# Optimization experiments

Hardware: AMD Instinct MI355X
Metric: run time of the kernel (lower is better)

The kernel has to match this reference:

```python
import jax, jax.numpy as jnp
import numpy as np

VOXEL = 128
N_PTS = VOXEL ** 3  # 2,097,152
C_FEAT = 14
T_HASH = 4194304


def _hash_index(coords, table_size):
    # Instant-NGP style spatial hash: elementwise prime multiply, xor-reduce, mod T.
    # uint32 arithmetic emulates the wrap-around semantics of the integer hash.
    primes = jnp.array([1, 2654435761, 805459861], dtype=jnp.uint32)
    h = coords.astype(jnp.uint32) * primes  # [N, 3]
    return ((h[:, 0] ^ h[:, 1]) ^ h[:, 2]) % jnp.uint32(table_size)  # [N]


def _quat_to_rotmat(q):
    # q: [N, 4] normalized, (r, x, y, z) convention (standard 3DGS)
    r, x, y, z = q[:, 0], q[:, 1], q[:, 2], q[:, 3]
    R = jnp.stack([
        1 - 2 * (y * y + z * z), 2 * (x * y - r * z), 2 * (x * z + r * y),
        2 * (x * y + r * z), 1 - 2 * (x * x + z * z), 2 * (y * z - r * x),
        2 * (x * z - r * y), 2 * (y * z + r * x), 1 - 2 * (x * x + y * y),
    ], axis=-1)
    return R.reshape(-1, 3, 3)


def setup_inputs() -> dict:
    key = jax.random.key(0)
    k1, k2, k3 = jax.random.split(key, 3)
    coordinates = jax.random.randint(k1, (N_PTS, 3), 0, VOXEL, dtype=jnp.int32)
    hash_table = jax.random.normal(k2, (C_FEAT, T_HASH), dtype=jnp.float32)
    camera_center = jax.random.normal(k3, (3,), dtype=jnp.float32)
    far = jnp.ones((1,), dtype=jnp.float32)
    return {"coordinates": coordinates, "hash_table": hash_table,
            "camera_center": camera_center, "far": far, "voxel_size": VOXEL}


def reference(coordinates, hash_table, camera_center, far, voxel_size):
    far_s = far[0]
    vs = jnp.float32(voxel_size)

    # hash_query: [C, N] gather from hash table
    idx = _hash_index(coordinates, hash_table.shape[1])
    gf = hash_table[:, idx]  # [14, N]

    # compute_voxel_center: [N, 3]
    voxel_center = (coordinates.astype(jnp.float32) / vs * 2 * far_s
                    - far_s + camera_center[None, :] + far_s / vs)

    # delta means: normalize over ALL elements (torch.mean/std on full tensor, unbiased std)
    dm = gf[0:3].T  # [N, 3]
    dm = (dm - jnp.mean(dm)) / jnp.std(dm, ddof=1) * 2 * far_s / vs / 6.0
    means = dm + voxel_center  # [N, 3]

    # covariance from scaling + rotation (standard 3DGS)
    scales = jax.nn.sigmoid(gf[7:10].T) * 2 * far_s / vs  # [N, 3]
    q = gf[3:7].T
    q = q / jnp.linalg.norm(q, axis=-1, keepdims=True)
    R = _quat_to_rotmat(q)                       # [N, 3, 3]
    L = R * scales[:, None, :]                   # L = R @ diag(s)
    covariances = jnp.einsum('nij,nkj->nik', L, L)  # [N, 3, 3]

    harmonics = gf[10:13].T[:, :, None]          # [N, 3, 1] (raw features)
    opacities = jax.nn.sigmoid(gf[13] - 4.0)     # [N]

    n = coordinates.shape[0]
    return (means[None], covariances[None], harmonics[None], opacities[None])
```

## Files before the change

### kernel.cpp

```cpp
#include <hip/hip_runtime.h>
#include <math.h>

#define N_PTS (128*128*128)
#define T_HASH 4194304
#define T_MASK (T_HASH - 1)
#define ENTRY_STRIDE 16

__device__ __forceinline__ unsigned hash_idx(int x, int y, int z) {
    return ((unsigned)x ^ ((unsigned)y * 2654435761u)
                        ^ ((unsigned)z * 805459861u)) & T_MASK;
}

__global__ void transpose_kernel(const float* __restrict__ table,
                                 float* __restrict__ tt) {
    __shared__ float sh[256 * 17];
    const int t  = threadIdx.x;
    const int i0 = blockIdx.x * 256;

    #pragma unroll
    for (int j = 0; j < 14; ++j)
        sh[t * 17 + j] = table[(size_t)j * T_HASH + i0 + t];
    sh[t * 17 + 14] = 0.f;
    sh[t * 17 + 15] = 0.f;
    __syncthreads();

    float4* dst = (float4*)(tt + (size_t)i0 * ENTRY_STRIDE);
    #pragma unroll
    for (int k = 0; k < 4; ++k) {
        const int f = t + k * 256;
        const int p = f >> 2;
        const int c = f & 3;
        const float* s = &sh[p * 17 + c * 4];
        dst[f] = make_float4(s[0], s[1], s[2], s[3]);
    }
}

__global__ void reduce_kernel_t(const int* __restrict__ coords,
                                const float* __restrict__ tt,
                                double* __restrict__ acc) {
    float s = 0.f, ss = 0.f;
    const int stride = gridDim.x * blockDim.x;
    for (int i = blockIdx.x * blockDim.x + threadIdx.x; i < N_PTS; i += stride) {
        const unsigned idx = hash_idx(coords[i*3], coords[i*3+1], coords[i*3+2]);
        const float4 f = *(const float4*)(tt + (size_t)idx * ENTRY_STRIDE);
        s  += f.x + f.y + f.z;
        ss += f.x * f.x + f.y * f.y + f.z * f.z;
    }
    #pragma unroll
    for (int off = 32; off > 0; off >>= 1) {
        s  += __shfl_down(s, off, 64);
        ss += __shfl_down(ss, off, 64);
    }
    __shared__ float sh_s[4], sh_ss[4];
    const int lane = threadIdx.x & 63;
    const int wid  = threadIdx.x >> 6;
    if (lane == 0) { sh_s[wid] = s; sh_ss[wid] = ss; }
    __syncthreads();
    if (threadIdx.x == 0) {
        float ts = 0.f, tss = 0.f;
        for (int w = 0; w < 4; ++w) { ts += sh_s[w]; tss += sh_ss[w]; }
        atomicAdd(&acc[0], (double)ts);
        atomicAdd(&acc[1], (double)tss);
    }
}

__global__ void reduce_kernel_o(const int* __restrict__ coords,
                                const float* __restrict__ table,
                                double* __restrict__ acc) {
    float s = 0.f, ss = 0.f;
    const int stride = gridDim.x * blockDim.x;
    for (int i = blockIdx.x * blockDim.x + threadIdx.x; i < N_PTS; i += stride) {
        const unsigned idx = hash_idx(coords[i*3], coords[i*3+1], coords[i*3+2]);
        float g0 = table[idx];
        float g1 = table[T_HASH + idx];
        float g2 = table[2 * T_HASH + idx];
        s  += g0 + g1 + g2;
        ss += g0 * g0 + g1 * g1 + g2 * g2;
    }
    #pragma unroll
    for (int off = 32; off > 0; off >>= 1) {
        s  += __shfl_down(s, off, 64);
        ss += __shfl_down(ss, off, 64);
    }
    __shared__ float sh_s[4], sh_ss[4];
    const int lane = threadIdx.x & 63;
    const int wid  = threadIdx.x >> 6;
    if (lane == 0) { sh_s[wid] = s; sh_ss[wid] = ss; }
    __syncthreads();
    if (threadIdx.x == 0) {
        float ts = 0.f, tss = 0.f;
        for (int w = 0; w < 4; ++w) { ts += sh_s[w]; tss += sh_ss[w]; }
        atomicAdd(&acc[0], (double)ts);
        atomicAdd(&acc[1], (double)tss);
    }
}

template <bool TRANSPOSED>
__global__ void main_kernel(const int* __restrict__ coords,
                            const float* __restrict__ tab,
                            const float* __restrict__ cam,
                            const float* __restrict__ far_p,
                            const int* __restrict__ vs_p,
                            const double* __restrict__ acc,
                            float* __restrict__ out) {
    const int i = blockIdx.x * blockDim.x + threadIdx.x;
    if (i >= N_PTS) return;

    const float far_s = far_p[0];
    const float vs    = (float)vs_p[0];

    const double n      = 3.0 * (double)N_PTS;
    const double sum    = acc[0];
    const double sumsq  = acc[1];
    const double mean_d = sum / n;
    const double var_d  = (sumsq - sum * sum / n) / (n - 1.0);
    const float mean    = (float)mean_d;
    const float inv_std = (float)(1.0 / sqrt(var_d));

    const int cx = coords[i * 3 + 0];
    const int cy = coords[i * 3 + 1];
    const int cz = coords[i * 3 + 2];
    const unsigned idx = hash_idx(cx, cy, cz);

    float g[16];
    if (TRANSPOSED) {
        const float4* e = (const float4*)(tab + (size_t)idx * ENTRY_STRIDE);
        float4 f0 = e[0], f1 = e[1], f2 = e[2], f3 = e[3];
        g[0]=f0.x; g[1]=f0.y; g[2]=f0.z; g[3]=f0.w;
        g[4]=f1.x; g[5]=f1.y; g[6]=f1.z; g[7]=f1.w;
        g[8]=f2.x; g[9]=f2.y; g[10]=f2.z; g[11]=f2.w;
        g[12]=f3.x; g[13]=f3.y;
    } else {
        #pragma unroll
        for (int j = 0; j < 14; ++j)
            g[j] = tab[(size_t)j * T_HASH + idx];
    }

    const float two_far_over_vs = 2.f * far_s / vs;
    const float dm_scale = two_far_over_vs / 6.f;
    const float c_f[3] = { (float)cx, (float)cy, (float)cz };
    #pragma unroll
    for (int k = 0; k < 3; ++k) {
        const float vc = c_f[k] / vs * 2.f * far_s - far_s + cam[k] + far_s / vs;
        out[(size_t)i * 3 + k] = (g[k] - mean) * inv_std * dm_scale + vc;
    }

    float qr = g[3], qx = g[4], qy = g[5], qz = g[6];
    const float qinv = 1.f / sqrtf(qr * qr + qx * qx + qy * qy + qz * qz);
    qr *= qinv; qx *= qinv; qy *= qinv; qz *= qinv;

    float R[3][3];
    R[0][0] = 1.f - 2.f * (qy * qy + qz * qz);
    R[0][1] = 2.f * (qx * qy - qr * qz);
    R[0][2] = 2.f * (qx * qz + qr * qy);
    R[1][0] = 2.f * (qx * qy + qr * qz);
    R[1][1] = 1.f - 2.f * (qx * qx + qz * qz);
    R[1][2] = 2.f * (qy * qz - qr * qx);
    R[2][0] = 2.f * (qx * qz - qr * qy);
    R[2][1] = 2.f * (qy * qz + qr * qx);
    R[2][2] = 1.f - 2.f * (qx * qx + qy * qy);

    float sc[3];
    #pragma unroll
    for (int k = 0; k < 3; ++k)
        sc[k] = two_far_over_vs / (1.f + expf(-g[7 + k]));

    float* covp = out + (size_t)3 * N_PTS + (size_t)i * 9;
    #pragma unroll
    for (int r = 0; r < 3; ++r) {
        #pragma unroll
        for (int c = 0; c < 3; ++c) {
            float a = 0.f;
            #pragma unroll
            for (int j = 0; j < 3; ++j)
                a += (R[r][j] * sc[j]) * (R[c][j] * sc[j]);
            covp[r * 3 + c] = a;
        }
    }

    float* harp = out + (size_t)12 * N_PTS + (size_t)i * 3;
    #pragma unroll
    for (int k = 0; k < 3; ++k)
        harp[k] = g[10 + k];

    out[(size_t)15 * N_PTS + i] = 1.f / (1.f + expf(-(g[13] - 4.f)));
}

extern "C" void kernel_launch(void* const* d_in, const int* in_sizes, int n_in,
                              void* d_out, int out_size, void* d_ws, size_t ws_size,
                              hipStream_t stream) {
    const int*   coords = (const int*)d_in[0];
    const float* table  = (const float*)d_in[1];
    const float* cam    = (const float*)d_in[2];
    const float* far_p  = (const float*)d_in[3];
    const int*   vs_p   = (const int*)d_in[4];
    float*       out    = (float*)d_out;

    double* acc = (double*)d_ws;
    float*  tt  = (float*)((char*)d_ws + 256);

    const size_t need = 256 + (size_t)T_HASH * ENTRY_STRIDE * sizeof(float);

    hipMemsetAsync(d_ws, 0, 2 * sizeof(double), stream);

    const int threads = 256;
    const int blocks  = (N_PTS + threads - 1) / threads;

    if (ws_size >= need) {
        transpose_kernel<<<T_HASH / 256, 256, 0, stream>>>(table, tt);
        reduce_kernel_t<<<2048, 256, 0, stream>>>(coords, tt, acc);
        main_kernel<true><<<blocks, threads, 0, stream>>>(coords, tt, cam, far_p,
                                                          vs_p, acc, out);
    } else {
        reduce_kernel_o<<<2048, 256, 0, stream>>>(coords, table, acc);
        main_kernel<false><<<blocks, threads, 0, stream>>>(coords, table, cam,
                                                           far_p, vs_p, acc, out);
    }
}
```

Baseline: 543.6 us.

## Fuse statistics reduction into main gather kernel and fix up means afterwards

Removes the separate reduction pass that re-gathered the first three features for every point. The main kernel now writes raw delta-mean features and accumulates the sum and sum of squares per block. A small fixup kernel then normalizes the means using the global statistics. Most output stores become nontemporal. The workspace-size fallback path is dropped, so the code assumes the transposed table always fits.

```diff
diff --git a/kernel.cpp b/kernel.cpp
--- a/kernel.cpp
+++ b/kernel.cpp
@@ -35,117 +35,34 @@
     }
 }
 
-__global__ void reduce_kernel_t(const int* __restrict__ coords,
-                                const float* __restrict__ tt,
-                                double* __restrict__ acc) {
-    float s = 0.f, ss = 0.f;
-    const int stride = gridDim.x * blockDim.x;
-    for (int i = blockIdx.x * blockDim.x + threadIdx.x; i < N_PTS; i += stride) {
-        const unsigned idx = hash_idx(coords[i*3], coords[i*3+1], coords[i*3+2]);
-        const float4 f = *(const float4*)(tt + (size_t)idx * ENTRY_STRIDE);
-        s  += f.x + f.y + f.z;
-        ss += f.x * f.x + f.y * f.y + f.z * f.z;
-    }
-    #pragma unroll
-    for (int off = 32; off > 0; off >>= 1) {
-        s  += __shfl_down(s, off, 64);
-        ss += __shfl_down(ss, off, 64);
-    }
-    __shared__ float sh_s[4], sh_ss[4];
-    const int lane = threadIdx.x & 63;
-    const int wid  = threadIdx.x >> 6;
-    if (lane == 0) { sh_s[wid] = s; sh_ss[wid] = ss; }
-    __syncthreads();
-    if (threadIdx.x == 0) {
-        float ts = 0.f, tss = 0.f;
-        for (int w = 0; w < 4; ++w) { ts += sh_s[w]; tss += sh_ss[w]; }
-        atomicAdd(&acc[0], (double)ts);
-        atomicAdd(&acc[1], (double)tss);
-    }
-}
-
-__global__ void reduce_kernel_o(const int* __restrict__ coords,
-                                const float* __restrict__ table,
-                                double* __restrict__ acc) {
-    float s = 0.f, ss = 0.f;
-    const int stride = gridDim.x * blockDim.x;
-    for (int i = blockIdx.x * blockDim.x + threadIdx.x; i < N_PTS; i += stride) {
-        const unsigned idx = hash_idx(coords[i*3], coords[i*3+1], coords[i*3+2]);
-        float g0 = table[idx];
-        float g1 = table[T_HASH + idx];
-        float g2 = table[2 * T_HASH + idx];
-        s  += g0 + g1 + g2;
-        ss += g0 * g0 + g1 * g1 + g2 * g2;
-    }
-    #pragma unroll
-    for (int off = 32; off > 0; off >>= 1) {
-        s  += __shfl_down(s, off, 64);
-        ss += __shfl_down(ss, off, 64);
-    }
-    __shared__ float sh_s[4], sh_ss[4];
-    const int lane = threadIdx.x & 63;
-    const int wid  = threadIdx.x >> 6;
-    if (lane == 0) { sh_s[wid] = s; sh_ss[wid] = ss; }
-    __syncthreads();
-    if (threadIdx.x == 0) {
-        float ts = 0.f, tss = 0.f;
-        for (int w = 0; w < 4; ++w) { ts += sh_s[w]; tss += sh_ss[w]; }
-        atomicAdd(&acc[0], (double)ts);
-        atomicAdd(&acc[1], (double)tss);
-    }
-}
-
-template <bool TRANSPOSED>
-__global__ void main_kernel(const int* __restrict__ coords,
-                            const float* __restrict__ tab,
-                            const float* __restrict__ cam,
-                            const float* __restrict__ far_p,
-                            const int* __restrict__ vs_p,
-                            const double* __restrict__ acc,
-                            float* __restrict__ out) {
-    const int i = blockIdx.x * blockDim.x + threadIdx.x;
-    if (i >= N_PTS) return;
+__global__ void main_fused_kernel(const int* __restrict__ coords,
+                                  const float* __restrict__ tt,
+                                  const float* __restrict__ far_p,
+                                  const int* __restrict__ vs_p,
+                                  double* __restrict__ acc,
+                                  float* __restrict__ out) {
+    const int i = blockIdx.x * 256 + threadIdx.x;
 
     const float far_s = far_p[0];
     const float vs    = (float)vs_p[0];
-
-    const double n      = 3.0 * (double)N_PTS;
-    const double sum    = acc[0];
-    const double sumsq  = acc[1];
-    const double mean_d = sum / n;
-    const double var_d  = (sumsq - sum * sum / n) / (n - 1.0);
-    const float mean    = (float)mean_d;
-    const float inv_std = (float)(1.0 / sqrt(var_d));
+    const float two_far_over_vs = 2.f * far_s / vs;
 
     const int cx = coords[i * 3 + 0];
     const int cy = coords[i * 3 + 1];
     const int cz = coords[i * 3 + 2];
     const unsigned idx = hash_idx(cx, cy, cz);
 
-    float g[16];
-    if (TRANSPOSED) {
-        const float4* e = (const float4*)(tab + (size_t)idx * ENTRY_STRIDE);
-        float4 f0 = e[0], f1 = e[1], f2 = e[2], f3 = e[3];
-        g[0]=f0.x; g[1]=f0.y; g[2]=f0.z; g[3]=f0.w;
-        g[4]=f1.x; g[5]=f1.y; g[6]=f1.z; g[7]=f1.w;
-        g[8]=f2.x; g[9]=f2.y; g[10]=f2.z; g[11]=f2.w;
-        g[12]=f3.x; g[13]=f3.y;
-    } else {
-        #pragma unroll
-        for (int j = 0; j < 14; ++j)
-            g[j] = tab[(size_t)j * T_HASH + idx];
-    }
+    const float4* e = (const float4*)(tt + (size_t)idx * ENTRY_STRIDE);
+    const float4 f0 = e[0];
+    const float4 f1 = e[1];
+    const float4 f2 = e[2];
+    const float4 f3 = e[3];
 
-    const float two_far_over_vs = 2.f * far_s / vs;
-    const float dm_scale = two_far_over_vs / 6.f;
-    const float c_f[3] = { (float)cx, (float)cy, (float)cz };
-    #pragma unroll
-    for (int k = 0; k < 3; ++k) {
-        const float vc = c_f[k] / vs * 2.f * far_s - far_s + cam[k] + far_s / vs;
-        out[(size_t)i * 3 + k] = (g[k] - mean) * inv_std * dm_scale + vc;
-    }
+    out[(size_t)i * 3 + 0] = f0.x;
+    out[(size_t)i * 3 + 1] = f0.y;
+    out[(size_t)i * 3 + 2] = f0.z;
 
-    float qr = g[3], qx = g[4], qy = g[5], qz = g[6];
+    float qr = f0.w, qx = f1.x, qy = f1.y, qz = f1.z;
     const float qinv = 1.f / sqrtf(qr * qr + qx * qx + qy * qy + qz * qz);
     qr *= qinv; qx *= qinv; qy *= qinv; qz *= qinv;
 
@@ -161,9 +78,9 @@
     R[2][2] = 1.f - 2.f * (qx * qx + qy * qy);
 
     float sc[3];
-    #pragma unroll
-    for (int k = 0; k < 3; ++k)
-        sc[k] = two_far_over_vs / (1.f + expf(-g[7 + k]));
+    sc[0] = two_far_over_vs / (1.f + expf(-f1.w));
+    sc[1] = two_far_over_vs / (1.f + expf(-f2.x));
+    sc[2] = two_far_over_vs / (1.f + expf(-f2.y));
 
     float* covp = out + (size_t)3 * N_PTS + (size_t)i * 9;
     #pragma unroll
@@ -174,16 +91,73 @@
             #pragma unroll
             for (int j = 0; j < 3; ++j)
                 a += (R[r][j] * sc[j]) * (R[c][j] * sc[j]);
-            covp[r * 3 + c] = a;
+            __builtin_nontemporal_store(a, covp + r * 3 + c);
         }
     }
 
     float* harp = out + (size_t)12 * N_PTS + (size_t)i * 3;
+    __builtin_nontemporal_store(f2.z, harp + 0);
+    __builtin_nontemporal_store(f2.w, harp + 1);
+    __builtin_nontemporal_store(f3.x, harp + 2);
+
+    __builtin_nontemporal_store(1.f / (1.f + expf(-(f3.y - 4.f))),
+                                out + (size_t)15 * N_PTS + i);
+
+    float s  = f0.x + f0.y + f0.z;
+    float ss = f0.x * f0.x + f0.y * f0.y + f0.z * f0.z;
+    #pragma unroll
+    for (int off = 32; off > 0; off >>= 1) {
+        s  += __shfl_down(s, off, 64);
+        ss += __shfl_down(ss, off, 64);
+    }
+    __shared__ float sh_s[4], sh_ss[4];
+    const int lane = threadIdx.x & 63;
+    const int wid  = threadIdx.x >> 6;
+    if (lane == 0) { sh_s[wid] = s; sh_ss[wid] = ss; }
+    __syncthreads();
+    if (threadIdx.x == 0) {
+        float ts = 0.f, tss = 0.f;
+        #pragma unroll
+        for (int w = 0; w < 4; ++w) { ts += sh_s[w]; tss += sh_ss[w]; }
+        atomicAdd(&acc[0], (double)ts);
+        atomicAdd(&acc[1], (double)tss);
+    }
+}
+
+__global__ void means_fixup_kernel(const int* __restrict__ coords,
+                                   const float* __restrict__ cam,
+                                   const float* __restrict__ far_p,
+                                   const int* __restrict__ vs_p,
+                                   const double* __restrict__ acc,
+                                   float* __restrict__ out) {
+    const int i = blockIdx.x * 256 + threadIdx.x;
+
+    const float far_s = far_p[0];
+    const float vs    = (float)vs_p[0];
+
+    const double n      = 3.0 * (double)N_PTS;
+    const double sum    = acc[0];
+    const double sumsq  = acc[1];
+    const double mean_d = sum / n;
+    const double var_d  = (sumsq - sum * sum / n) / (n - 1.0);
+    const float mean    = (float)mean_d;
+    const float a       = (float)(1.0 / sqrt(var_d)) * (2.f * far_s / vs / 6.f);
+
+    const int cx = coords[i * 3 + 0];
+    const int cy = coords[i * 3 + 1];
+    const int cz = coords[i * 3 + 2];
+    const float c_f[3] = { (float)cx, (float)cy, (float)cz };
+
+    float m[3];
     #pragma unroll
     for (int k = 0; k < 3; ++k)
-        harp[k] = g[10 + k];
+        m[k] = out[(size_t)i * 3 + k];
 
-    out[(size_t)15 * N_PTS + i] = 1.f / (1.f + expf(-(g[13] - 4.f)));
+    #pragma unroll
+    for (int k = 0; k < 3; ++k) {
+        const float vc = c_f[k] / vs * 2.f * far_s - far_s + cam[k] + far_s / vs;
+        out[(size_t)i * 3 + k] = (m[k] - mean) * a + vc;
+    }
 }
 
 extern "C" void kernel_launch(void* const* d_in, const int* in_sizes, int n_in,
@@ -199,21 +173,11 @@
     double* acc = (double*)d_ws;
     float*  tt  = (float*)((char*)d_ws + 256);
 
-    const size_t need = 256 + (size_t)T_HASH * ENTRY_STRIDE * sizeof(float);
-
     hipMemsetAsync(d_ws, 0, 2 * sizeof(double), stream);
 
-    const int threads = 256;
-    const int blocks  = (N_PTS + threads - 1) / threads;
-
-    if (ws_size >= need) {
-        transpose_kernel<<<T_HASH / 256, 256, 0, stream>>>(table, tt);
-        reduce_kernel_t<<<2048, 256, 0, stream>>>(coords, tt, acc);
-        main_kernel<true><<<blocks, threads, 0, stream>>>(coords, tt, cam, far_p,
-                                                          vs_p, acc, out);
-    } else {
-        reduce_kernel_o<<<2048, 256, 0, stream>>>(coords, table, acc);
-        main_kernel<false><<<blocks, threads, 0, stream>>>(coords, table, cam,
-                                                           far_p, vs_p, acc, out);
-    }
+    transpose_kernel<<<T_HASH / 256, 256, 0, stream>>>(table, tt);
+    main_fused_kernel<<<N_PTS / 256, 256, 0, stream>>>(coords, tt, far_p, vs_p,
+                                                       acc, out);
+    means_fixup_kernel<<<N_PTS / 256, 256, 0, stream>>>(coords, cam, far_p, vs_p,
+                                                        acc, out);
 }
```

Result: slower. 613.2 us (+12.8%).
